# Kernel tuning notes

Hardware: AMD Instinct MI355X
Metric: run time of the kernel (lower is better)

## Reference

```python
import jax, jax.numpy as jnp
import numpy as np

N_NODES = 100000
N_EDGES = 1600000
IN_CH, HID_CH, OUT_CH = 128, 128, 2


def setup_inputs() -> dict:
    key = jax.random.key(0)
    k1, k2, k3, k4 = jax.random.split(key, 4)
    x = jax.random.normal(k1, (N_NODES, IN_CH), dtype=jnp.float32)
    edge_index = jax.random.randint(k2, (2, N_EDGES), 0, N_NODES, dtype=jnp.int64)
    # Glorot-ish init for GCNConv weights, zero bias (PyG default)
    W1 = jax.random.normal(k3, (IN_CH, HID_CH), dtype=jnp.float32) / np.sqrt(IN_CH)
    b1 = jnp.zeros((HID_CH,), dtype=jnp.float32)
    W2 = jax.random.normal(k4, (HID_CH, OUT_CH), dtype=jnp.float32) / np.sqrt(HID_CH)
    b2 = jnp.zeros((OUT_CH,), dtype=jnp.float32)
    return {"x": x, "edge_index": edge_index, "W1": W1, "b1": b1, "W2": W2, "b2": b2}


def _gcn_conv(x, W, b, src, dst, deg_inv_sqrt, n_nodes):
    # PyG GCNConv: transform, then symmetric-normalized aggregation with self-loops.
    xw = x @ W  # [N, F_out]
    norm = deg_inv_sqrt[src] * deg_inv_sqrt[dst]  # [E]
    agg = jax.ops.segment_sum(xw[src] * norm[:, None], dst, num_segments=n_nodes)
    # self-loop contribution: norm_ii = deg_inv_sqrt[i]^2
    agg = agg + xw * (deg_inv_sqrt * deg_inv_sqrt)[:, None]
    return agg + b


def reference(x, edge_index, W1, b1, W2, b2):
    src, dst = edge_index[0], edge_index[1]
    n = x.shape[0]
    # degree of A + I (in-degree at dst, +1 for self-loop)
    deg = jax.ops.segment_sum(jnp.ones_like(dst, dtype=x.dtype), dst, num_segments=n) + 1.0
    deg_inv_sqrt = jax.lax.rsqrt(deg)
    h = _gcn_conv(x, W1, b1, src, dst, deg_inv_sqrt, n)
    h = jax.nn.relu(h)
    out = _gcn_conv(h, W2, b2, src, dst, deg_inv_sqrt, n)
    return out
```

## Files before the change

### kernel.cpp

```cpp
#include <hip/hip_runtime.h>

#define N_NODES 100000
#define N_EDGES 1600000
#define B_COARSE 196
#define NODES_PER_CB 512
#define CAP_C 9216
#define EPB 4096
#define NBLK_SCAT ((N_EDGES + EPB - 1) / EPB)

__device__ __forceinline__ int clamp_idx(int v) {
  return v < 0 ? 0 : (v >= N_NODES ? N_NODES - 1 : v);
}

__device__ __forceinline__ unsigned short f2bf(float f) {
  unsigned u = __float_as_uint(f);
  unsigned r = ((u >> 16) & 1u) + 0x7fffu;
  return (unsigned short)((u + r) >> 16);
}
__device__ __forceinline__ float bf_lo(unsigned u) { return __uint_as_float(u << 16); }
__device__ __forceinline__ float bf_hi(unsigned u) { return __uint_as_float(u & 0xffff0000u); }

__global__ __launch_bounds__(1024) void scatter_coarse(const int* __restrict__ src,
                                                       const int* __restrict__ dst,
                                                       int* __restrict__ cursor,
                                                       int* __restrict__ eraw) {
  __shared__ int lhist[B_COARSE];
  __shared__ int lscan[B_COARSE];
  __shared__ int lbase[B_COARSE];
  __shared__ int lrec[EPB];
  __shared__ short lbkt[EPB];
  int tid = threadIdx.x;
  int e0 = blockIdx.x * EPB;
  for (int i = tid; i < B_COARSE; i += 1024) lhist[i] = 0;
  __syncthreads();
  int myrec[4], myb[4], mypos[4];
#pragma unroll
  for (int k = 0; k < 4; ++k) {
    int e = e0 + k * 1024 + tid;
    bool v = e < N_EDGES;
    int s = v ? clamp_idx(src[e]) : 0;
    int d = v ? clamp_idx(dst[e]) : 0;
    int b = d >> 9;
    myrec[k] = s | ((d & 511) << 20);
    myb[k] = b;
    mypos[k] = v ? atomicAdd(&lhist[b], 1) : -1;
  }
  __syncthreads();
  if (tid < 64) {
    int carry = 0;
    for (int c = 0; c < B_COARSE; c += 64) {
      int idx = c + tid;
      int v = (idx < B_COARSE) ? lhist[idx] : 0;
      int x = v;
#pragma unroll
      for (int dlt = 1; dlt < 64; dlt <<= 1) {
        int y = __shfl_up(x, dlt);
        if (tid >= dlt) x += y;
      }
      if (idx < B_COARSE) lscan[idx] = carry + x - v;
      carry += __shfl(x, 63);
    }
  }
  __syncthreads();
  if (tid < B_COARSE) {
    int cnt = lhist[tid];
    lbase[tid] = cnt > 0 ? atomicAdd(&cursor[tid], cnt) : 0;
  }
#pragma unroll
  for (int k = 0; k < 4; ++k) {
    if (mypos[k] >= 0) {
      int p = lscan[myb[k]] + mypos[k];
      lrec[p] = myrec[k];
      lbkt[p] = (short)myb[k];
    }
  }
  __syncthreads();
  int tot = lscan[B_COARSE - 1] + lhist[B_COARSE - 1];
  for (int i = tid; i < tot; i += 1024) {
    int b = lbkt[i];
    int p = lbase[b] + (i - lscan[b]);
    if (p < CAP_C) eraw[b * CAP_C + p] = lrec[i];
  }
}

__global__ __launch_bounds__(1024) void bucket_sort(const int* __restrict__ cursor,
                                                    const int* __restrict__ eraw,
                                                    int* __restrict__ esrt,
                                                    int* __restrict__ row_start,
                                                    int* __restrict__ counts,
                                                    float* __restrict__ dis) {
  __shared__ int lhist[NODES_PER_CB];
  __shared__ int lcur[NODES_PER_CB];
  __shared__ int lplaced[CAP_C];
  int cb = blockIdx.x;
  int tid = threadIdx.x;
  int cnt = cursor[cb];
  cnt = cnt > CAP_C ? CAP_C : cnt;
  const int* base = &eraw[cb * CAP_C];
  for (int i = tid; i < NODES_PER_CB; i += 1024) lhist[i] = 0;
  __syncthreads();
  for (int i = tid; i < cnt; i += 1024) {
    atomicAdd(&lhist[base[i] >> 20], 1);
  }
  __syncthreads();
  if (tid < 64) {
    int carry = 0;
    for (int c = 0; c < NODES_PER_CB; c += 64) {
      int idx = c + tid;
      int v = lhist[idx];
      int x = v;
#pragma unroll
      for (int dlt = 1; dlt < 64; dlt <<= 1) {
        int y = __shfl_up(x, dlt);
        if (tid >= dlt) x += y;
      }
      lcur[idx] = carry + x - v;
      carry += __shfl(x, 63);
    }
  }
  __syncthreads();
  if (tid < NODES_PER_CB) {
    int n = cb * NODES_PER_CB + tid;
    if (n < N_NODES) {
      int v = lhist[tid];
      counts[n] = v;
      row_start[n] = cb * CAP_C + lcur[tid];
      dis[n] = rsqrtf((float)v + 1.0f);
    }
  }
  __syncthreads();
  for (int i = tid; i < cnt; i += 1024) {
    int r = base[i];
    int pos = atomicAdd(&lcur[r >> 20], 1);
    lplaced[pos] = r & 0xFFFFF;
  }
  __syncthreads();
  for (int i = tid; i < cnt; i += 1024) {
    esrt[cb * CAP_C + i] = lplaced[i];
  }
}

__global__ __launch_bounds__(256) void gemm_xw(const float* __restrict__ x,
                                               const float* __restrict__ Wg,
                                               const float* __restrict__ dis,
                                               unsigned int* __restrict__ xwb) {
  __shared__ float Wl[32 * 128];
  __shared__ float Xlt[32 * 36];
  int t = threadIdx.x;
  int r0 = blockIdx.x * 32;
  int tx = t & 31, ty = t >> 5;
  float acc[4][4] = {};

  for (int kb = 0; kb < 4; ++kb) {
    __syncthreads();
#pragma unroll
    for (int i = 0; i < 4; ++i) {
      int f = (i * 256 + t) * 4;
      *(float4*)&Wl[f] = *(const float4*)&Wg[kb * 32 * 128 + f];
    }
    {
      int row = t >> 3, kk = (t & 7) * 4;
      float4 v = *(const float4*)&x[(r0 + row) * 128 + kb * 32 + kk];
      Xlt[(kk + 0) * 36 + row] = v.x;
      Xlt[(kk + 1) * 36 + row] = v.y;
      Xlt[(kk + 2) * 36 + row] = v.z;
      Xlt[(kk + 3) * 36 + row] = v.w;
    }
    __syncthreads();
#pragma unroll
    for (int k = 0; k < 32; ++k) {
      float4 wv = *(float4*)&Wl[k * 128 + tx * 4];
      float4 xv = *(float4*)&Xlt[k * 36 + ty * 4];
      float xr[4] = {xv.x, xv.y, xv.z, xv.w};
#pragma unroll
      for (int i = 0; i < 4; ++i) {
        acc[i][0] += xr[i] * wv.x;
        acc[i][1] += xr[i] * wv.y;
        acc[i][2] += xr[i] * wv.z;
        acc[i][3] += xr[i] * wv.w;
      }
    }
  }
#pragma unroll
  for (int i = 0; i < 4; ++i) {
    int row = r0 + ty * 4 + i;
    float dsc = dis[row];
    unsigned lo = ((unsigned)f2bf(acc[i][1] * dsc) << 16) | f2bf(acc[i][0] * dsc);
    unsigned hi = ((unsigned)f2bf(acc[i][3] * dsc) << 16) | f2bf(acc[i][2] * dsc);
    *(uint2*)&xwb[row * 64 + tx * 2] = make_uint2(lo, hi);
  }
}

__global__ __launch_bounds__(256) void agg1_kernel(const unsigned int* __restrict__ xwb,
                                                   const float* __restrict__ b1,
                                                   const float* __restrict__ W2,
                                                   const float* __restrict__ dis,
                                                   const int* __restrict__ row_start,
                                                   const int* __restrict__ counts,
                                                   const int* __restrict__ esrt,
                                                   float* __restrict__ hws) {
  int wid = blockIdx.x * 4 + (threadIdx.x >> 6);
  if (wid >= N_NODES) return;
  int lane = threadIdx.x & 63;
  int q = lane >> 4;
  int sub = lane & 15;
  int c = sub * 8;
  int start = row_start[wid];
  int cnt = counts[wid];
  const uint4* xw4 = (const uint4*)xwb;

  float a0 = 0.f, a1 = 0.f, a2 = 0.f, a3 = 0.f;
  float a4 = 0.f, a5 = 0.f, a6 = 0.f, a7 = 0.f;

  int full = cnt & ~15;
  for (int i = 0; i < full; i += 16) {
#pragma unroll
    for (int k = 0; k < 4; ++k) {
      int s = esrt[start + i + 4 * k + q];
      uint4 g = xw4[s * 16 + sub];
      a0 += bf_lo(g.x); a1 += bf_hi(g.x);
      a2 += bf_lo(g.y); a3 += bf_hi(g.y);
      a4 += bf_lo(g.z); a5 += bf_hi(g.z);
      a6 += bf_lo(g.w); a7 += bf_hi(g.w);
    }
  }
  if (full < cnt) {
#pragma unroll
    for (int k = 0; k < 4; ++k) {
      int ei = full + 4 * k + q;
      bool valid = ei < cnt;
      int s = esrt[valid ? (start + ei) : start];
      float n = valid ? 1.0f : 0.0f;
      uint4 g = xw4[s * 16 + sub];
      a0 += bf_lo(g.x) * n; a1 += bf_hi(g.x) * n;
      a2 += bf_lo(g.y) * n; a3 += bf_hi(g.y) * n;
      a4 += bf_lo(g.z) * n; a5 += bf_hi(g.z) * n;
      a6 += bf_lo(g.w) * n; a7 += bf_hi(g.w) * n;
    }
  }
  a0 += __shfl_xor(a0, 16); a1 += __shfl_xor(a1, 16);
  a2 += __shfl_xor(a2, 16); a3 += __shfl_xor(a3, 16);
  a4 += __shfl_xor(a4, 16); a5 += __shfl_xor(a5, 16);
  a6 += __shfl_xor(a6, 16); a7 += __shfl_xor(a7, 16);
  a0 += __shfl_xor(a0, 32); a1 += __shfl_xor(a1, 32);
  a2 += __shfl_xor(a2, 32); a3 += __shfl_xor(a3, 32);
  a4 += __shfl_xor(a4, 32); a5 += __shfl_xor(a5, 32);
  a6 += __shfl_xor(a6, 32); a7 += __shfl_xor(a7, 32);

  float disw = dis[wid];
  uint4 gs = xw4[wid * 16 + sub];
  a0 += bf_lo(gs.x); a1 += bf_hi(gs.x);
  a2 += bf_lo(gs.y); a3 += bf_hi(gs.y);
  a4 += bf_lo(gs.z); a5 += bf_hi(gs.z);
  a6 += bf_lo(gs.w); a7 += bf_hi(gs.w);
  float4 bv0 = *(const float4*)&b1[c];
  float4 bv1 = *(const float4*)&b1[c + 4];
  a0 = fmaxf(fmaf(a0, disw, bv0.x), 0.f);
  a1 = fmaxf(fmaf(a1, disw, bv0.y), 0.f);
  a2 = fmaxf(fmaf(a2, disw, bv0.z), 0.f);
  a3 = fmaxf(fmaf(a3, disw, bv0.w), 0.f);
  a4 = fmaxf(fmaf(a4, disw, bv1.x), 0.f);
  a5 = fmaxf(fmaf(a5, disw, bv1.y), 0.f);
  a6 = fmaxf(fmaf(a6, disw, bv1.z), 0.f);
  a7 = fmaxf(fmaf(a7, disw, bv1.w), 0.f);

  float4 wA = *(const float4*)&W2[c * 2];
  float4 wB = *(const float4*)&W2[c * 2 + 4];
  float4 wC = *(const float4*)&W2[c * 2 + 8];
  float4 wD = *(const float4*)&W2[c * 2 + 12];
  float p0 = a0 * wA.x + a1 * wA.z + a2 * wB.x + a3 * wB.z +
             a4 * wC.x + a5 * wC.z + a6 * wD.x + a7 * wD.z;
  float p1 = a0 * wA.y + a1 * wA.w + a2 * wB.y + a3 * wB.w +
             a4 * wC.y + a5 * wC.w + a6 * wD.y + a7 * wD.w;
#pragma unroll
  for (int off = 8; off >= 1; off >>= 1) {
    p0 += __shfl_xor(p0, off);
    p1 += __shfl_xor(p1, off);
  }
  if (lane == 0) *(float2*)&hws[wid * 2] = make_float2(p0 * disw, p1 * disw);
}

__global__ __launch_bounds__(256) void agg2_kernel(const float* __restrict__ hws,
                                                   const float* __restrict__ b2,
                                                   const float* __restrict__ dis,
                                                   const int* __restrict__ row_start,
                                                   const int* __restrict__ counts,
                                                   const int* __restrict__ esrt,
                                                   float* __restrict__ out) {
  int tid = threadIdx.x;
  int wid = blockIdx.x * 16 + (tid >> 4);
  if (wid >= N_NODES) return;
  int sub = tid & 15;
  int start = row_start[wid];
  int cnt = counts[wid];
  float a0 = 0.f, a1 = 0.f;
  for (int i = sub; i < cnt; i += 16) {
    int s = esrt[start + i];
    float2 v = *(const float2*)&hws[s * 2];
    a0 += v.x;
    a1 += v.y;
  }
#pragma unroll
  for (int off = 8; off >= 1; off >>= 1) {
    a0 += __shfl_xor(a0, off);
    a1 += __shfl_xor(a1, off);
  }
  if (sub == 0) {
    float disw = dis[wid];
    float2 vd = *(const float2*)&hws[wid * 2];
    out[wid * 2 + 0] = fmaf(a0 + vd.x, disw, b2[0]);
    out[wid * 2 + 1] = fmaf(a1 + vd.y, disw, b2[1]);
  }
}


extern "C" void kernel_launch(void* const* d_in, const int* in_sizes, int n_in,
                              void* d_out, int out_size, void* d_ws, size_t ws_size,
                              hipStream_t stream) {
  const float* x  = (const float*)d_in[0];
  const int*   ei = (const int*)d_in[1];
  const float* W1 = (const float*)d_in[2];
  const float* b1 = (const float*)d_in[3];
  const float* W2 = (const float*)d_in[4];
  const float* b2 = (const float*)d_in[5];
  float* out = (float*)d_out;

  const int* src = ei;
  const int* dst = ei + N_EDGES;

  char* ws = (char*)d_ws;
  size_t off = 0;
  auto walloc = [&](size_t bytes) -> void* {
    void* p = ws + off;
    off += (bytes + 255) & ~(size_t)255;
    return p;
  };
  unsigned int* xwb = (unsigned int*)walloc((size_t)N_NODES * 128 * 2);
  int*   cursor     = (int*)walloc((size_t)B_COARSE * 4);
  int*   eraw       = (int*)walloc((size_t)B_COARSE * CAP_C * 4);
  int*   esrt       = (int*)walloc((size_t)B_COARSE * CAP_C * 4);
  int*   row_start  = (int*)walloc((size_t)N_NODES * 4);
  int*   counts     = (int*)walloc((size_t)N_NODES * 4);
  float* dis        = (float*)walloc((size_t)N_NODES * 4);
  float* hws        = (float*)walloc((size_t)N_NODES * 2 * 4);

  if (off > ws_size) return;

  hipMemsetAsync(cursor, 0, (size_t)B_COARSE * 4, stream);

  scatter_coarse<<<NBLK_SCAT, 1024, 0, stream>>>(src, dst, cursor, eraw);
  bucket_sort<<<B_COARSE, 1024, 0, stream>>>(cursor, eraw, esrt, row_start, counts, dis);
  gemm_xw<<<N_NODES / 32, 256, 0, stream>>>(x, W1, dis, xwb);
  agg1_kernel<<<(N_NODES + 3) / 4, 256, 0, stream>>>(xwb, b1, W2, dis, row_start, counts,
                                                     esrt, hws);
  agg2_kernel<<<(N_NODES + 15) / 16, 256, 0, stream>>>(hws, b2, dis, row_start, counts,
                                                       esrt, out);
}
```

Measured before the change: 237.4 us.

## Replace FP32 SIMT X·W1 GEMM with bf16 MFMA kernel and prepacked W1 fragments

The first-layer feature transform moves from a scalar FP32 shared-memory GEMM to matrix-core MFMA 16x16x32 bf16 instructions. A small one-block kernel pre-packs W1 into per-lane bf16 fragments. The GEMM converts x to bf16 in LDS, runs the MFMA, scales rows by the degree normalizer, and writes bf16 output through LDS as coalesced stores. The aim is to cut the GEMM's compute time. The cost is an extra kernel launch and bf16 rounding of the inputs, where before only the outputs were rounded.

```diff
diff --git a/kernel.cpp b/kernel.cpp
--- a/kernel.cpp
+++ b/kernel.cpp
@@ -7,6 +7,9 @@
 #define CAP_C 9216
 #define EPB 4096
 #define NBLK_SCAT ((N_EDGES + EPB - 1) / EPB)
+
+typedef __attribute__((ext_vector_type(8))) short bf16x8;
+typedef __attribute__((ext_vector_type(4))) float f32x4;
 
 __device__ __forceinline__ int clamp_idx(int v) {
   return v < 0 ? 0 : (v >= N_NODES ? N_NODES - 1 : v);
@@ -140,54 +143,96 @@
   }
 }
 
-__global__ __launch_bounds__(256) void gemm_xw(const float* __restrict__ x,
-                                               const float* __restrict__ Wg,
-                                               const float* __restrict__ dis,
-                                               unsigned int* __restrict__ xwb) {
-  __shared__ float Wl[32 * 128];
-  __shared__ float Xlt[32 * 36];
+__global__ __launch_bounds__(256) void w1frag_kernel(const float* __restrict__ W1,
+                                                     unsigned int* __restrict__ w1f) {
   int t = threadIdx.x;
-  int r0 = blockIdx.x * 32;
-  int tx = t & 31, ty = t >> 5;
-  float acc[4][4] = {};
-
-  for (int kb = 0; kb < 4; ++kb) {
-    __syncthreads();
-#pragma unroll
-    for (int i = 0; i < 4; ++i) {
-      int f = (i * 256 + t) * 4;
-      *(float4*)&Wl[f] = *(const float4*)&Wg[kb * 32 * 128 + f];
-    }
-    {
-      int row = t >> 3, kk = (t & 7) * 4;
-      float4 v = *(const float4*)&x[(r0 + row) * 128 + kb * 32 + kk];
-      Xlt[(kk + 0) * 36 + row] = v.x;
-      Xlt[(kk + 1) * 36 + row] = v.y;
-      Xlt[(kk + 2) * 36 + row] = v.z;
-      Xlt[(kk + 3) * 36 + row] = v.w;
-    }
-    __syncthreads();
-#pragma unroll
-    for (int k = 0; k < 32; ++k) {
-      float4 wv = *(float4*)&Wl[k * 128 + tx * 4];
-      float4 xv = *(float4*)&Xlt[k * 36 + ty * 4];
-      float xr[4] = {xv.x, xv.y, xv.z, xv.w};
-#pragma unroll
-      for (int i = 0; i < 4; ++i) {
-        acc[i][0] += xr[i] * wv.x;
-        acc[i][1] += xr[i] * wv.y;
-        acc[i][2] += xr[i] * wv.z;
-        acc[i][3] += xr[i] * wv.w;
-      }
-    }
-  }
-#pragma unroll
-  for (int i = 0; i < 4; ++i) {
-    int row = r0 + ty * 4 + i;
-    float dsc = dis[row];
-    unsigned lo = ((unsigned)f2bf(acc[i][1] * dsc) << 16) | f2bf(acc[i][0] * dsc);
-    unsigned hi = ((unsigned)f2bf(acc[i][3] * dsc) << 16) | f2bf(acc[i][2] * dsc);
-    *(uint2*)&xwb[row * 64 + tx * 2] = make_uint2(lo, hi);
+#pragma unroll
+  for (int it = 0; it < 8; ++it) {
+    int slot = it * 256 + t;
+    int kt = slot >> 9;
+    int nt = (slot >> 6) & 7;
+    int lane = slot & 63;
+    int col = nt * 16 + (lane & 15);
+    int kbase = kt * 32 + (lane >> 4) * 8;
+    unsigned u[4];
+#pragma unroll
+    for (int jj = 0; jj < 4; ++jj) {
+      float f0 = W1[(kbase + 2 * jj) * 128 + col];
+      float f1 = W1[(kbase + 2 * jj + 1) * 128 + col];
+      u[jj] = ((unsigned)f2bf(f1) << 16) | f2bf(f0);
+    }
+    *(uint4*)&w1f[slot * 4] = make_uint4(u[0], u[1], u[2], u[3]);
+  }
+}
+
+__global__ __launch_bounds__(256) void gemm_mfma(const float* __restrict__ x,
+                                                 const unsigned int* __restrict__ w1f,
+                                                 const float* __restrict__ dis,
+                                                 unsigned int* __restrict__ xwb) {
+  __shared__ unsigned short Sl[64 * 136];
+  unsigned int* Xl = (unsigned int*)Sl;
+  int t = threadIdx.x;
+  int r0 = blockIdx.x * 64;
+  int w = t >> 6, lane = t & 63;
+
+#pragma unroll
+  for (int it = 0; it < 8; ++it) {
+    int flat = it * 256 + t;
+    int row = flat >> 5;
+    int c4 = flat & 31;
+    int grow = r0 + row;
+    float4 v = (grow < N_NODES) ? *(const float4*)&x[grow * 128 + c4 * 4]
+                                : make_float4(0.f, 0.f, 0.f, 0.f);
+    unsigned lo = ((unsigned)f2bf(v.y) << 16) | f2bf(v.x);
+    unsigned hi = ((unsigned)f2bf(v.w) << 16) | f2bf(v.z);
+    *(uint2*)&Xl[row * 68 + c4 * 2] = make_uint2(lo, hi);
+  }
+  __syncthreads();
+
+  f32x4 acc[8];
+#pragma unroll
+  for (int nt = 0; nt < 8; ++nt) acc[nt] = (f32x4){0.f, 0.f, 0.f, 0.f};
+
+  int lrow = (w << 4) + (lane & 15);
+#pragma unroll
+  for (int kt = 0; kt < 4; ++kt) {
+    int cu = (kt * 4 + (lane >> 4)) * 4;
+    bf16x8 af = *(const bf16x8*)&Xl[lrow * 68 + cu];
+#pragma unroll
+    for (int nt = 0; nt < 8; ++nt) {
+      bf16x8 bfr = *(const bf16x8*)&w1f[((kt * 8 + nt) * 64 + lane) * 4];
+      acc[nt] = __builtin_amdgcn_mfma_f32_16x16x32_bf16(af, bfr, acc[nt], 0, 0, 0);
+    }
+  }
+  __syncthreads();
+
+  float dsc[4];
+#pragma unroll
+  for (int reg = 0; reg < 4; ++reg) {
+    int grow = r0 + (w << 4) + ((lane >> 4) << 2) + reg;
+    dsc[reg] = (grow < N_NODES) ? dis[grow] : 0.f;
+  }
+#pragma unroll
+  for (int nt = 0; nt < 8; ++nt) {
+#pragma unroll
+    for (int reg = 0; reg < 4; ++reg) {
+      int lr = (w << 4) + ((lane >> 4) << 2) + reg;
+      int col = nt * 16 + (lane & 15);
+      Sl[lr * 136 + col] = f2bf(acc[nt][reg] * dsc[reg]);
+    }
+  }
+  __syncthreads();
+
+#pragma unroll
+  for (int it = 0; it < 4; ++it) {
+    int flat = it * 256 + t;
+    int row = flat >> 4;
+    int c = flat & 15;
+    int grow = r0 + row;
+    if (grow < N_NODES) {
+      uint4 v = *(uint4*)&Xl[row * 68 + c * 4];
+      *(uint4*)&xwb[grow * 64 + c * 4] = v;
+    }
   }
 }
 
@@ -343,14 +388,16 @@
   int*   counts     = (int*)walloc((size_t)N_NODES * 4);
   float* dis        = (float*)walloc((size_t)N_NODES * 4);
   float* hws        = (float*)walloc((size_t)N_NODES * 2 * 4);
+  unsigned int* w1f = (unsigned int*)walloc((size_t)2048 * 16);
 
   if (off > ws_size) return;
 
   hipMemsetAsync(cursor, 0, (size_t)B_COARSE * 4, stream);
 
+  w1frag_kernel<<<1, 256, 0, stream>>>(W1, w1f);
   scatter_coarse<<<NBLK_SCAT, 1024, 0, stream>>>(src, dst, cursor, eraw);
   bucket_sort<<<B_COARSE, 1024, 0, stream>>>(cursor, eraw, esrt, row_start, counts, dis);
-  gemm_xw<<<N_NODES / 32, 256, 0, stream>>>(x, W1, dis, xwb);
+  gemm_mfma<<<(N_NODES + 63) / 64, 256, 0, stream>>>(x, w1f, dis, xwb);
   agg1_kernel<<<(N_NODES + 3) / 4, 256, 0, stream>>>(xwb, b1, W2, dis, row_start, counts,
                                                      esrt, hws);
   agg2_kernel<<<(N_NODES + 15) / 16, 256, 0, stream>>>(hws, b2, dis, row_start, counts,
```

Result: faster. 209.8 us (-11.6%).
